# Kernel tuning notes

Hardware: AMD Instinct MI355X
Metric: run time of the kernel (lower is better)

Reference implementation:

```python
import jax, jax.numpy as jnp
import numpy as np

N = 100000
E = 3200000
D = 256


def setup_inputs() -> dict:
    key = jax.random.key(0)
    k1, k2, k3, k4 = jax.random.split(key, 4)
    x = jax.random.normal(k1, (N, D), dtype=jnp.float32)
    edge_index = jax.random.randint(k2, (2, E), 0, N, dtype=jnp.int64)
    # Glorot-ish scale for weights
    s = 1.0 / np.sqrt(D)
    W1 = jax.random.normal(k3, (D, D), dtype=jnp.float32) * s
    W2 = jax.random.normal(k4, (D, D), dtype=jnp.float32) * s
    b1 = jnp.zeros((D,), dtype=jnp.float32)
    b2 = jnp.zeros((D,), dtype=jnp.float32)
    return {"x": x, "edge_index": edge_index, "W1": W1, "b1": b1, "W2": W2, "b2": b2}


def _gcn_norm(edge_index, num_nodes):
    # PyG gcn_norm with add_self_loops=True, symmetric normalization.
    loop = jnp.arange(num_nodes, dtype=edge_index.dtype)
    src = jnp.concatenate([edge_index[0], loop])  # [E+N]
    dst = jnp.concatenate([edge_index[1], loop])  # [E+N]
    ones = jnp.ones(src.shape[0], dtype=jnp.float32)
    deg = jax.ops.segment_sum(ones, dst, num_segments=num_nodes)  # in-degree incl. self loop
    dis = jnp.where(deg > 0, jax.lax.rsqrt(deg), 0.0)
    norm = dis[src] * dis[dst]  # [E+N]
    return src, dst, norm


def _gcn_layer(x, src, dst, norm, W, b, num_nodes):
    xw = x @ W                                   # [N, D] dense GEMM
    msg = xw[src] * norm[:, None]                # gather + scale  [E+N, D]
    out = jax.ops.segment_sum(msg, dst, num_segments=num_nodes)  # scatter-add
    return out + b


def reference(x, edge_index, W1, b1, W2, b2):
    src, dst, norm = _gcn_norm(edge_index, N)
    h = jax.nn.elu(_gcn_layer(x, src, dst, norm, W1, b1, N))
    h = jax.nn.elu(_gcn_layer(h, src, dst, norm, W2, b2, N))
    return h
```

## Files before the change

kernel.cpp:

```cpp
#include <hip/hip_runtime.h>
#include <math.h>

#define N_NODES 100000
#define N_EDGES 3200000
#define DIM 256
#define SCAN_B 1024
#define SCAN_NBLK ((N_NODES + SCAN_B - 1) / SCAN_B)

typedef unsigned short u16;
typedef unsigned int u32;
typedef __attribute__((ext_vector_type(8))) short bf16x8;
typedef __attribute__((ext_vector_type(4))) float f32x4;

__device__ __forceinline__ float bf2f(u16 u) {
    union { u32 i; float f; } v; v.i = ((u32)u) << 16; return v.f;
}
__device__ __forceinline__ u16 f2bf(float f) {
    union { float f; u32 i; } v; v.f = f;
    u32 x = v.i;
    return (u16)((x + 0x7fffu + ((x >> 16) & 1u)) >> 16);
}
__device__ __forceinline__ float sane(float v) {
    union { float f; u32 i; } u; u.f = v;
    if ((u.i & 0x7f800000u) == 0x7f800000u) return 0.f;
    return v;
}
__device__ __forceinline__ int iclamp(int v, int lo, int hi) {
    return v < lo ? lo : (v > hi ? hi : v);
}

__global__ void detect_kernel(const u32* __restrict__ xw_words,
                              const int* __restrict__ ei, int* __restrict__ flags) {
    int lane = threadIdx.x;
    int cnt = 0;
#pragma unroll
    for (int j = 0; j < 4; ++j) {
        u32 e = (xw_words[lane + 64 * j] >> 7) & 0xffu;
        cnt += (e >= 0x70 && e <= 0x88) ? 1 : 0;
    }
    int nz = 0;
#pragma unroll
    for (int j = 0; j < 4; ++j) nz += (ei[2 * (lane + 64 * j) + 1] != 0) ? 1 : 0;
#pragma unroll
    for (int off = 32; off; off >>= 1) {
        cnt += __shfl_down(cnt, off, 64);
        nz += __shfl_down(nz, off, 64);
    }
    if (lane == 0) {
        flags[0] = (cnt < 128) ? 1 : 0;
        flags[1] = (nz == 0) ? 1 : 0;
    }
}

__device__ __forceinline__ int edge_val(const int* __restrict__ ei, int which,
                                        int i, int f64) {
    long long idx = (long long)which * N_EDGES + i;
    int v = f64 ? ei[idx * 2] : ei[idx];
    return iclamp(v, 0, N_NODES - 1);
}

__global__ void convert_x(const void* __restrict__ xin, u16* __restrict__ xbf,
                          const int* __restrict__ flags) {
    long long i = (long long)blockIdx.x * blockDim.x + threadIdx.x;
    if (i >= (long long)N_NODES * DIM) return;
    float v = flags[0] ? ((const float*)xin)[i] : bf2f(((const u16*)xin)[i]);
    xbf[i] = f2bf(sane(v));
}

__global__ void count_deg(const int* __restrict__ ei, int* __restrict__ rowcount,
                          const int* __restrict__ flags) {
    int i = blockIdx.x * blockDim.x + threadIdx.x;
    if (i < N_EDGES) {
        int d = edge_val(ei, 1, i, flags[1]);
        atomicAdd(&rowcount[d], 1);
    }
}

__global__ void compute_dis(const int* __restrict__ rowcount, float* __restrict__ dis) {
    int i = blockIdx.x * blockDim.x + threadIdx.x;
    if (i < N_NODES) {
        int c = iclamp(rowcount[i], 0, N_EDGES);
        dis[i] = rsqrtf((float)(c + 1));
    }
}

__global__ __launch_bounds__(SCAN_B) void scan_block_sums(const int* __restrict__ cnt,
                                                          int* __restrict__ bsum) {
    __shared__ int ws[16];
    int i = blockIdx.x * SCAN_B + threadIdx.x;
    int v = (i < N_NODES) ? cnt[i] : 0;
#pragma unroll
    for (int off = 32; off; off >>= 1) v += __shfl_down(v, off, 64);
    if ((threadIdx.x & 63) == 0) ws[threadIdx.x >> 6] = v;
    __syncthreads();
    if (threadIdx.x < 16) {
        int t = ws[threadIdx.x];
#pragma unroll
        for (int off = 8; off; off >>= 1) t += __shfl_down(t, off, 16);
        if (threadIdx.x == 0) bsum[blockIdx.x] = t;
    }
}

__global__ void scan_bsum(int* __restrict__ bsum, int* __restrict__ rowptr) {
    __shared__ int sdata[128];
    int i = threadIdx.x;
    int v = (i < SCAN_NBLK) ? bsum[i] : 0;
    sdata[i] = v;
    __syncthreads();
    for (int off = 1; off < 128; off <<= 1) {
        int t = (i >= off) ? sdata[i - off] : 0;
        __syncthreads();
        sdata[i] += t;
        __syncthreads();
    }
    if (i < SCAN_NBLK) bsum[i] = sdata[i] - v;
    if (i == 0) rowptr[N_NODES] = sdata[127];
}

__global__ __launch_bounds__(SCAN_B) void scan_final(const int* __restrict__ cnt,
                                                     const int* __restrict__ bsum,
                                                     int* __restrict__ rowptr,
                                                     int* __restrict__ cursor) {
    __shared__ int ws[16];
    int lane = threadIdx.x & 63;
    int wid = threadIdx.x >> 6;
    int i = blockIdx.x * SCAN_B + threadIdx.x;
    int c = (i < N_NODES) ? cnt[i] : 0;
    int v = c;
#pragma unroll
    for (int off = 1; off < 64; off <<= 1) {
        int t = __shfl_up(v, off, 64);
        if (lane >= off) v += t;
    }
    if (lane == 63) ws[wid] = v;
    __syncthreads();
    int woff = 0;
    for (int w = 0; w < wid; ++w) woff += ws[w];
    int excl = bsum[blockIdx.x] + woff + v - c;
    if (i < N_NODES) { rowptr[i] = excl; cursor[i] = excl; }
}

__global__ void fill_csr(const int* __restrict__ ei, int* __restrict__ cursor,
                         int* __restrict__ colidx, const int* __restrict__ flags) {
    int i = blockIdx.x * blockDim.x + threadIdx.x;
    if (i < N_EDGES) {
        int f = flags[1];
        int s = edge_val(ei, 0, i, f);
        int d = edge_val(ei, 1, i, f);
        int pos = atomicAdd(&cursor[d], 1);
        colidx[pos] = s;
    }
}

__global__ void transpose_w(const void* __restrict__ W, u16* __restrict__ Wt,
                            const int* __restrict__ flags) {
    int n = blockIdx.x;
    int k = threadIdx.x;
    float v = flags[0] ? ((const float*)W)[k * DIM + n]
                       : bf2f(((const u16*)W)[k * DIM + n]);
    Wt[n * DIM + k] = f2bf(sane(v));
}

__global__ __launch_bounds__(256) void gemm_mfma(const u16* __restrict__ A,
                                                 const u16* __restrict__ Wt,
                                                 u16* __restrict__ out, int M) {
    int wid = threadIdx.x >> 6;
    int lane = threadIdx.x & 63;
    int rt = blockIdx.x * 4 + wid;
    if (rt * 16 >= M) return;
    int m = lane & 15;
    int quad = lane >> 4;
    const u16* arow = A + (size_t)(rt * 16 + m) * DIM + quad * 8;

    f32x4 acc[16];
#pragma unroll
    for (int t = 0; t < 16; ++t) acc[t] = (f32x4){0.f, 0.f, 0.f, 0.f};

#pragma unroll
    for (int ks = 0; ks < 8; ++ks) {
        bf16x8 a = *(const bf16x8*)(arow + ks * 32);
#pragma unroll
        for (int t = 0; t < 16; ++t) {
            bf16x8 b = *(const bf16x8*)(Wt + (size_t)(t * 16 + m) * DIM + ks * 32 + quad * 8);
            acc[t] = __builtin_amdgcn_mfma_f32_16x16x32_bf16(a, b, acc[t], 0, 0, 0);
        }
    }
#pragma unroll
    for (int t = 0; t < 16; ++t) {
#pragma unroll
        for (int r = 0; r < 4; ++r) {
            int row = rt * 16 + quad * 4 + r;
            int c = t * 16 + m;
            out[(size_t)row * DIM + c] = f2bf(sane(acc[t][r]));
        }
    }
}

__global__ __launch_bounds__(256) void aggregate(const u16* __restrict__ xw,
                                                 const int* __restrict__ rowptr,
                                                 const int* __restrict__ colidx,
                                                 const float* __restrict__ dis,
                                                 const void* __restrict__ bias,
                                                 void* __restrict__ out,
                                                 const int* __restrict__ flags,
                                                 int final_layer) {
    int wid = threadIdx.x >> 6;
    int lane = threadIdx.x & 63;
    int node = blockIdx.x * 4 + wid;
    if (node >= N_NODES) return;
    int c0 = lane * 4;
    const u16* base = xw + c0;

    float dn = dis[node];
    float a0, a1, a2, a3;
    {
        ushort4 v = *(const ushort4*)(base + (size_t)node * DIM);
        a0 = dn * bf2f(v.x); a1 = dn * bf2f(v.y);
        a2 = dn * bf2f(v.z); a3 = dn * bf2f(v.w);
    }
    int beg = rowptr[node];
    int end = rowptr[node + 1];
    int e = beg;
    for (; e + 8 <= end; e += 8) {
        int s[8];
        float w[8];
        ushort4 vv[8];
#pragma unroll
        for (int k = 0; k < 8; ++k) s[k] = colidx[e + k];
#pragma unroll
        for (int k = 0; k < 8; ++k) vv[k] = *(const ushort4*)(base + (size_t)s[k] * DIM);
#pragma unroll
        for (int k = 0; k < 8; ++k) w[k] = dis[s[k]];
#pragma unroll
        for (int k = 0; k < 8; ++k) {
            a0 += w[k] * bf2f(vv[k].x);
            a1 += w[k] * bf2f(vv[k].y);
            a2 += w[k] * bf2f(vv[k].z);
            a3 += w[k] * bf2f(vv[k].w);
        }
    }
    for (; e < end; ++e) {
        int s = colidx[e];
        float w = dis[s];
        ushort4 v = *(const ushort4*)(base + (size_t)s * DIM);
        a0 += w * bf2f(v.x); a1 += w * bf2f(v.y);
        a2 += w * bf2f(v.z); a3 += w * bf2f(v.w);
    }

    float b0, b1, b2, b3;
    int f32mode = flags[0];
    if (f32mode) {
        float4 bv = *(const float4*)((const float*)bias + c0);
        b0 = bv.x; b1 = bv.y; b2 = bv.z; b3 = bv.w;
    } else {
        ushort4 bv = *(const ushort4*)((const u16*)bias + c0);
        b0 = bf2f(bv.x); b1 = bf2f(bv.y); b2 = bf2f(bv.z); b3 = bf2f(bv.w);
    }
    float o0 = dn * a0 + b0;
    float o1 = dn * a1 + b1;
    float o2 = dn * a2 + b2;
    float o3 = dn * a3 + b3;
    o0 = sane(o0 > 0.f ? o0 : expm1f(o0));
    o1 = sane(o1 > 0.f ? o1 : expm1f(o1));
    o2 = sane(o2 > 0.f ? o2 : expm1f(o2));
    o3 = sane(o3 > 0.f ? o3 : expm1f(o3));
    if (final_layer && f32mode) {
        float4 ov; ov.x = o0; ov.y = o1; ov.z = o2; ov.w = o3;
        *(float4*)((float*)out + (size_t)node * DIM + c0) = ov;
    } else {
        ushort4 ov;
        ov.x = f2bf(o0); ov.y = f2bf(o1); ov.z = f2bf(o2); ov.w = f2bf(o3);
        *(ushort4*)((u16*)out + (size_t)node * DIM + c0) = ov;
    }
}

extern "C" void kernel_launch(void* const* d_in, const int* in_sizes, int n_in,
                              void* d_out, int out_size, void* d_ws, size_t ws_size,
                              hipStream_t stream) {
    const void* x  = d_in[0];
    const int*  ei = (const int*)d_in[1];
    const void* W1 = d_in[2];
    const void* b1 = d_in[3];
    const void* W2 = d_in[4];
    const void* b2 = d_in[5];

    char* ws = (char*)d_ws;
    size_t off = 0;
    auto alloc = [&](size_t bytes) {
        void* p = ws + off;
        off = (off + bytes + 255) & ~(size_t)255;
        return p;
    };
    int*   flags    = (int*)alloc(256);
    int*   rowcount = (int*)alloc((size_t)N_NODES * 4);
    int*   rowptr   = (int*)alloc((size_t)(N_NODES + 1) * 4);
    int*   cursor   = (int*)alloc((size_t)N_NODES * 4);
    int*   colidx   = (int*)alloc((size_t)N_EDGES * 4);
    float* dis      = (float*)alloc((size_t)N_NODES * 4);
    int*   bsum     = (int*)alloc((size_t)SCAN_NBLK * 4 + 256);
    u16*   Wt       = (u16*)alloc((size_t)DIM * DIM * 2);
    u16*   xw       = (u16*)alloc((size_t)N_NODES * DIM * 2);
    (void)ws_size;

    u16* xbf = (u16*)d_out;

    detect_kernel<<<1, 64, 0, stream>>>((const u32*)x, ei, flags);
    hipMemsetAsync(rowcount, 0, (size_t)N_NODES * 4, stream);
    convert_x<<<(N_NODES * DIM + 255) / 256, 256, 0, stream>>>(x, xbf, flags);
    count_deg<<<(N_EDGES + 255) / 256, 256, 0, stream>>>(ei, rowcount, flags);
    compute_dis<<<(N_NODES + 255) / 256, 256, 0, stream>>>(rowcount, dis);
    scan_block_sums<<<SCAN_NBLK, SCAN_B, 0, stream>>>(rowcount, bsum);
    scan_bsum<<<1, 128, 0, stream>>>(bsum, rowptr);
    scan_final<<<SCAN_NBLK, SCAN_B, 0, stream>>>(rowcount, bsum, rowptr, cursor);
    fill_csr<<<(N_EDGES + 255) / 256, 256, 0, stream>>>(ei, cursor, colidx, flags);

    int gemm_blocks = (N_NODES / 16 + 3) / 4;

    transpose_w<<<DIM, DIM, 0, stream>>>(W1, Wt, flags);
    gemm_mfma<<<gemm_blocks, 256, 0, stream>>>(xbf, Wt, xw, N_NODES);
    aggregate<<<N_NODES / 4, 256, 0, stream>>>(xw, rowptr, colidx, dis, b1, d_out, flags, 0);

    transpose_w<<<DIM, DIM, 0, stream>>>(W2, Wt, flags);
    gemm_mfma<<<gemm_blocks, 256, 0, stream>>>((const u16*)d_out, Wt, xw, N_NODES);
    aggregate<<<N_NODES / 4, 256, 0, stream>>>(xw, rowptr, colidx, dis, b2, d_out, flags, 1);
}
```

Baseline: 1.302 ms.

## Windowed multi-pass CSR fill and register-resident weight tiles in GEMM

```diff
diff --git a/kernel.cpp b/kernel.cpp
--- a/kernel.cpp
+++ b/kernel.cpp
@@ -6,6 +6,8 @@
 #define DIM 256
 #define SCAN_B 1024
 #define SCAN_NBLK ((N_NODES + SCAN_B - 1) / SCAN_B)
+#define NPASS 8
+#define WIN ((N_NODES + NPASS - 1) / NPASS)
 
 typedef unsigned short u16;
 typedef unsigned int u32;
@@ -67,11 +69,16 @@
     xbf[i] = f2bf(sane(v));
 }
 
-__global__ void count_deg(const int* __restrict__ ei, int* __restrict__ rowcount,
-                          const int* __restrict__ flags) {
+__global__ void count_convert(const int* __restrict__ ei, int* __restrict__ rowcount,
+                              int* __restrict__ src32, int* __restrict__ dst32,
+                              const int* __restrict__ flags) {
     int i = blockIdx.x * blockDim.x + threadIdx.x;
     if (i < N_EDGES) {
-        int d = edge_val(ei, 1, i, flags[1]);
+        int f = flags[1];
+        int s = edge_val(ei, 0, i, f);
+        int d = edge_val(ei, 1, i, f);
+        src32[i] = s;
+        dst32[i] = d;
         atomicAdd(&rowcount[d], 1);
     }
 }
@@ -140,15 +147,17 @@
     if (i < N_NODES) { rowptr[i] = excl; cursor[i] = excl; }
 }
 
-__global__ void fill_csr(const int* __restrict__ ei, int* __restrict__ cursor,
-                         int* __restrict__ colidx, const int* __restrict__ flags) {
+__global__ void fill_csr_pass(const int* __restrict__ src32,
+                              const int* __restrict__ dst32,
+                              int* __restrict__ cursor, int* __restrict__ colidx,
+                              int lo) {
     int i = blockIdx.x * blockDim.x + threadIdx.x;
     if (i < N_EDGES) {
-        int f = flags[1];
-        int s = edge_val(ei, 0, i, f);
-        int d = edge_val(ei, 1, i, f);
-        int pos = atomicAdd(&cursor[d], 1);
-        colidx[pos] = s;
+        int d = dst32[i];
+        if ((unsigned)(d - lo) < (unsigned)WIN) {
+            int pos = atomicAdd(&cursor[d], 1);
+            colidx[pos] = src32[i];
+        }
     }
 }
 
@@ -163,35 +172,41 @@
 
 __global__ __launch_bounds__(256) void gemm_mfma(const u16* __restrict__ A,
                                                  const u16* __restrict__ Wt,
-                                                 u16* __restrict__ out, int M) {
-    int wid = threadIdx.x >> 6;
+                                                 u16* __restrict__ out) {
+    int w = threadIdx.x >> 6;
     int lane = threadIdx.x & 63;
-    int rt = blockIdx.x * 4 + wid;
-    if (rt * 16 >= M) return;
+    int rt = blockIdx.x;
     int m = lane & 15;
     int quad = lane >> 4;
+
+    bf16x8 B[4][8];
+#pragma unroll
+    for (int t2 = 0; t2 < 4; ++t2)
+#pragma unroll
+        for (int ks = 0; ks < 8; ++ks)
+            B[t2][ks] = *(const bf16x8*)(Wt + (size_t)((w * 4 + t2) * 16 + m) * DIM +
+                                         ks * 32 + quad * 8);
+
     const u16* arow = A + (size_t)(rt * 16 + m) * DIM + quad * 8;
-
-    f32x4 acc[16];
-#pragma unroll
-    for (int t = 0; t < 16; ++t) acc[t] = (f32x4){0.f, 0.f, 0.f, 0.f};
+    f32x4 acc[4];
+#pragma unroll
+    for (int t2 = 0; t2 < 4; ++t2) acc[t2] = (f32x4){0.f, 0.f, 0.f, 0.f};
 
 #pragma unroll
     for (int ks = 0; ks < 8; ++ks) {
         bf16x8 a = *(const bf16x8*)(arow + ks * 32);
 #pragma unroll
-        for (int t = 0; t < 16; ++t) {
-            bf16x8 b = *(const bf16x8*)(Wt + (size_t)(t * 16 + m) * DIM + ks * 32 + quad * 8);
-            acc[t] = __builtin_amdgcn_mfma_f32_16x16x32_bf16(a, b, acc[t], 0, 0, 0);
-        }
-    }
-#pragma unroll
-    for (int t = 0; t < 16; ++t) {
+        for (int t2 = 0; t2 < 4; ++t2)
+            acc[t2] = __builtin_amdgcn_mfma_f32_16x16x32_bf16(a, B[t2][ks], acc[t2], 0, 0, 0);
+    }
+
+#pragma unroll
+    for (int t2 = 0; t2 < 4; ++t2) {
 #pragma unroll
         for (int r = 0; r < 4; ++r) {
             int row = rt * 16 + quad * 4 + r;
-            int c = t * 16 + m;
-            out[(size_t)row * DIM + c] = f2bf(sane(acc[t][r]));
+            int c = w * 64 + t2 * 16 + m;
+            out[(size_t)row * DIM + c] = f2bf(sane(acc[t2][r]));
         }
     }
 }
@@ -302,25 +317,28 @@
     u16*   xw       = (u16*)alloc((size_t)N_NODES * DIM * 2);
     (void)ws_size;
 
+    int* src32 = (int*)xw;
+    int* dst32 = src32 + N_EDGES;
+
     u16* xbf = (u16*)d_out;
 
     detect_kernel<<<1, 64, 0, stream>>>((const u32*)x, ei, flags);
     hipMemsetAsync(rowcount, 0, (size_t)N_NODES * 4, stream);
-    convert_x<<<(N_NODES * DIM + 255) / 256, 256, 0, stream>>>(x, xbf, flags);
-    count_deg<<<(N_EDGES + 255) / 256, 256, 0, stream>>>(ei, rowcount, flags);
+    count_convert<<<(N_EDGES + 255) / 256, 256, 0, stream>>>(ei, rowcount, src32, dst32, flags);
     compute_dis<<<(N_NODES + 255) / 256, 256, 0, stream>>>(rowcount, dis);
     scan_block_sums<<<SCAN_NBLK, SCAN_B, 0, stream>>>(rowcount, bsum);
     scan_bsum<<<1, 128, 0, stream>>>(bsum, rowptr);
     scan_final<<<SCAN_NBLK, SCAN_B, 0, stream>>>(rowcount, bsum, rowptr, cursor);
-    fill_csr<<<(N_EDGES + 255) / 256, 256, 0, stream>>>(ei, cursor, colidx, flags);
-
-    int gemm_blocks = (N_NODES / 16 + 3) / 4;
+    for (int p = 0; p < NPASS; ++p)
+        fill_csr_pass<<<(N_EDGES + 255) / 256, 256, 0, stream>>>(src32, dst32, cursor,
+                                                                 colidx, p * WIN);
+    convert_x<<<(N_NODES * DIM + 255) / 256, 256, 0, stream>>>(x, xbf, flags);
 
     transpose_w<<<DIM, DIM, 0, stream>>>(W1, Wt, flags);
-    gemm_mfma<<<gemm_blocks, 256, 0, stream>>>(xbf, Wt, xw, N_NODES);
+    gemm_mfma<<<N_NODES / 16, 256, 0, stream>>>(xbf, Wt, xw);
     aggregate<<<N_NODES / 4, 256, 0, stream>>>(xw, rowptr, colidx, dis, b1, d_out, flags, 0);
 
     transpose_w<<<DIM, DIM, 0, stream>>>(W2, Wt, flags);
-    gemm_mfma<<<gemm_blocks, 256, 0, stream>>>((const u16*)d_out, Wt, xw, N_NODES);
+    gemm_mfma<<<N_NODES / 16, 256, 0, stream>>>((const u16*)d_out, Wt, xw);
     aggregate<<<N_NODES / 4, 256, 0, stream>>>(xw, rowptr, colidx, dis, b2, d_out, flags, 1);
 }
```

Result: faster. 1.236 ms (-5.1%).
